# Kernel tuning notes

Hardware: AMD Instinct MI355X
Metric: run time of the kernel (lower is better)

## Reference

```python
import jax, jax.numpy as jnp
import numpy as np

B, C, H, W = 4, 128, 64, 64
HEADS = 4
GROUPS = 32
EPS = 1e-5


def setup_inputs() -> dict:
    key = jax.random.key(0)
    ks = jax.random.split(key, 7)
    x = jax.random.normal(ks[0], (B, C, H, W), jnp.float32)
    gn_gamma = 1.0 + 0.1 * jax.random.normal(ks[1], (C,), jnp.float32)
    gn_beta = 0.1 * jax.random.normal(ks[2], (C,), jnp.float32)
    # 1x1 convs stored as [out_ch, in_ch]
    w_qkv = jax.random.normal(ks[3], (3 * C, C), jnp.float32) / np.sqrt(C).astype(np.float32)
    b_qkv = 0.02 * jax.random.normal(ks[4], (3 * C,), jnp.float32)
    # proj_out is zero-init in the original; use small random weights so the
    # full math path (not just the residual) is exercised.
    w_proj = jax.random.normal(ks[5], (C, C), jnp.float32) / np.sqrt(C).astype(np.float32)
    b_proj = 0.02 * jax.random.normal(ks[6], (C,), jnp.float32)
    return {"x": x, "gn_gamma": gn_gamma, "gn_beta": gn_beta,
            "w_qkv": w_qkv, "b_qkv": b_qkv, "w_proj": w_proj, "b_proj": b_proj}


def reference(x, gn_gamma, gn_beta, w_qkv, b_qkv, w_proj, b_proj):
    b, c, h, w = x.shape
    # GroupNorm(32, C, affine=True)
    xg = x.reshape(b, GROUPS, c // GROUPS, h, w)
    mean = xg.mean(axis=(2, 3, 4), keepdims=True)
    var = xg.var(axis=(2, 3, 4), keepdims=True)
    hn = ((xg - mean) * jax.lax.rsqrt(var + EPS)).reshape(b, c, h, w)
    hn = hn * gn_gamma[None, :, None, None] + gn_beta[None, :, None, None]
    # 1x1 conv -> qkv: [B, 3C, H, W]
    qkv = jnp.einsum('bchw,oc->bohw', hn, w_qkv) + b_qkv[None, :, None, None]
    L = h * w
    qkv = qkv.reshape(b, 3 * c, L)
    q, k, v = jnp.split(qkv, 3, axis=1)  # each [B, C, L]
    ch = c // HEADS
    scale = 1.0 / np.sqrt(np.sqrt(ch)).astype(np.float32)
    qh = (q * scale).reshape(b * HEADS, ch, L)
    kh = (k * scale).reshape(b * HEADS, ch, L)
    vh = v.reshape(b * HEADS, ch, L)
    # full [B*heads, L, L] score matrix (as in the original einsum path)
    weight = jnp.einsum('bct,bcs->bts', qh, kh)
    weight = jax.nn.softmax(weight.astype(jnp.float32), axis=-1).astype(qkv.dtype)
    a = jnp.einsum('bts,bcs->bct', weight, vh).reshape(b, c, h, w)
    out = jnp.einsum('bchw,oc->bohw', a, w_proj) + b_proj[None, :, None, None]
    return x + out
```

## Files before the change

kernel.cpp:

```cpp
#include <hip/hip_runtime.h>
#include <math.h>

#define B_ 4
#define C_ 128
#define L_ 4096
#define EPS_ 1e-5f

typedef __attribute__((ext_vector_type(8))) short short8;
typedef __attribute__((ext_vector_type(4))) float f32x4;
typedef __attribute__((ext_vector_type(16))) float f32x16;

static __device__ __forceinline__ unsigned short f2bf(float f) {
  union { float f; unsigned u; } v; v.f = f;
  return (unsigned short)((v.u + 0x7FFFu + ((v.u >> 16) & 1u)) >> 16);
}
static __device__ __forceinline__ f32x4 fzero() {
  f32x4 z; z[0] = 0.f; z[1] = 0.f; z[2] = 0.f; z[3] = 0.f; return z;
}
static __device__ __forceinline__ f32x16 zero16() {
  f32x16 z;
#pragma unroll
  for (int i = 0; i < 16; ++i) z[i] = 0.f;
  return z;
}
static __device__ __forceinline__ float fexp2(float x) {
  return __builtin_amdgcn_exp2f(x);
}
static __device__ __forceinline__ unsigned cvtpk(float lo, float hi) {
  unsigned r;
  asm("v_cvt_pk_bf16_f32 %0, %1, %2" : "=v"(r) : "v"(lo), "v"(hi));
  return r;
}
#define PLSWAP(a, b) asm("v_permlane32_swap_b32 %0, %1" : "+v"(a), "+v"(b))


__global__ __launch_bounds__(256) void gn_prep(const float* __restrict__ x,
                                               float* __restrict__ mean,
                                               float* __restrict__ rstd,
                                               const float* __restrict__ wqkv,
                                               const float* __restrict__ bqkv,
                                               const float* __restrict__ wproj,
                                               unsigned short* __restrict__ wqkv_bf,
                                               unsigned short* __restrict__ wproj_bf,
                                               float* __restrict__ bqkv_s) {
  int bx = blockIdx.x;
  int tid = threadIdx.x;
  if (bx < 128) {
    int g = bx & 31, b = bx >> 5;
    const f32x4* p4 = (const f32x4*)(x + (size_t)(b * C_ + g * 4) * L_);
    float s = 0.f, sq = 0.f;
#pragma unroll
    for (int i = 0; i < 16; ++i) {
      f32x4 v = p4[tid + i * 256];
      s += v[0] + v[1] + v[2] + v[3];
      sq += v[0]*v[0] + v[1]*v[1] + v[2]*v[2] + v[3]*v[3];
    }
#pragma unroll
    for (int m = 1; m < 64; m <<= 1) { s += __shfl_xor(s, m, 64); sq += __shfl_xor(sq, m, 64); }
    __shared__ float ls[8];
    int w = tid >> 6;
    if ((tid & 63) == 0) { ls[w] = s; ls[4 + w] = sq; }
    __syncthreads();
    if (tid == 0) {
      float S = ls[0] + ls[1] + ls[2] + ls[3];
      float Q = ls[4] + ls[5] + ls[6] + ls[7];
      float mu = S * (1.f / 16384.f);
      float var = Q * (1.f / 16384.f) - mu * mu;
      mean[b * 32 + g] = mu;
      rstd[b * 32 + g] = rsqrtf(var + EPS_);
    }
  } else {
    const float SC = 0.42044820762685725f * 1.2011224087864498f;
    int i = (bx - 128) * 256 + tid;
    if (i < 49152) {
      int o = i >> 7;
      wqkv_bf[i] = f2bf(wqkv[i] * (o < 256 ? SC : 1.f));
    } else if (i < 65536) {
      wproj_bf[i - 49152] = f2bf(wproj[i - 49152]);
    } else if (i < 65920) {
      int o = i - 65536;
      bqkv_s[o] = bqkv[o] * (o < 256 ? SC : 1.f);
    }
  }
}

__global__ __launch_bounds__(256) void qkv_gemm(const float* __restrict__ x,
                                                const float* __restrict__ gamma,
                                                const float* __restrict__ beta,
                                                const float* __restrict__ mean,
                                                const float* __restrict__ rstd,
                                                const unsigned short* __restrict__ wqkv_bf,
                                                const float* __restrict__ bqkv_s,
                                                unsigned short* __restrict__ qbuf,
                                                char* __restrict__ kf,
                                                char* __restrict__ vf) {
  __shared__ char lds[64 * 256];
  int b = blockIdx.y;
  int pos0 = blockIdx.x * 64;
  int tid = threadIdx.x;

#pragma unroll
  for (int it = 0; it < 4; ++it) {
    int pi = it * 256 + tid;
    int c = (pi >> 4) * 2;
    int pl = (pi & 15) * 4;
    const float* xc = x + (size_t)(b * C_ + c) * L_ + pos0 + pl;
    f32x4 v0 = *(const f32x4*)xc;
    f32x4 v1 = *(const f32x4*)(xc + L_);
    int g = c >> 2;
    float rs = rstd[b * 32 + g], mu = mean[b * 32 + g];
    float A0 = rs * gamma[c],     B0 = beta[c]     - mu * A0;
    float A1 = rs * gamma[c + 1], B1 = beta[c + 1] - mu * A1;
#pragma unroll
    for (int i = 0; i < 4; ++i) {
      int row = pl + i;
      unsigned u = cvtpk(v0[i] * A0 + B0, v1[i] * A1 + B1);
      *(unsigned*)(lds + row * 256 + ((c * 2) ^ ((row & 7) << 4))) = u;
    }
  }
  __syncthreads();

  int l = tid & 63, w = tid >> 6;
  int ln = l & 15, g4 = l >> 4;
  int lrow = w * 16 + ln;

  short8 afrag[4];
#pragma unroll
  for (int kc = 0; kc < 4; ++kc) {
    int col2 = (kc * 32 + g4 * 8) * 2;
    afrag[kc] = *(const short8*)(lds + lrow * 256 + (col2 ^ ((lrow & 7) << 4)));
  }

  f32x4 acc[24];
#pragma unroll
  for (int nt = 0; nt < 24; ++nt) acc[nt] = fzero();
#pragma unroll
  for (int nt = 0; nt < 24; ++nt) {
#pragma unroll
    for (int kc = 0; kc < 4; ++kc) {
      short8 bfrag = *(const short8*)(wqkv_bf + (size_t)(nt * 16 + ln) * 128 + kc * 32 + g4 * 8);
      acc[nt] = __builtin_amdgcn_mfma_f32_16x16x32_bf16(afrag[kc], bfrag, acc[nt], 0, 0, 0);
    }
  }

  int posb = pos0 + w * 16 + g4 * 4;
  int s_ = posb >> 5;
#pragma unroll
  for (int nt = 0; nt < 24; ++nt) {
    int o = nt * 16 + ln;
    float bias = bqkv_s[o];
    unsigned u01 = cvtpk(acc[nt][0] + bias, acc[nt][1] + bias);
    unsigned u23 = cvtpk(acc[nt][2] + bias, acc[nt][3] + bias);
    if (o < 128) {
      int bh = b * 4 + (o >> 5);
      unsigned short* p = qbuf + ((size_t)bh * L_ + posb) * 32 + (o & 31);
      p[0]  = (unsigned short)u01; p[32] = (unsigned short)(u01 >> 16);
      p[64] = (unsigned short)u23; p[96] = (unsigned short)(u23 >> 16);
    } else if (o < 256) {
      int o2 = o - 128;
      int bh = b * 4 + (o2 >> 5);
      int d = o2 & 31;
      int hi_ = (d >> 3) & 1, blk_ = d >> 4, j_ = d & 7;
      int lq0 = posb & 31;
      char* base = kf + (size_t)bh * 262144 + s_ * 2048 + blk_ * 1024 + j_ * 2
                 + (hi_ * 32 + lq0) * 16;
      *(unsigned short*)(base)      = (unsigned short)u01;
      *(unsigned short*)(base + 16) = (unsigned short)(u01 >> 16);
      *(unsigned short*)(base + 32) = (unsigned short)u23;
      *(unsigned short*)(base + 48) = (unsigned short)(u23 >> 16);
    } else {
      int ch = o - 256;
      int bh = b * 4 + (ch >> 5);
      int d = ch & 31;
      int r5 = posb & 31;
      int hi_ = (r5 >> 3) & 1, blk_ = (r5 >> 4) & 1, j0 = r5 & 7;
      char* addr = vf + (size_t)bh * 262144 + s_ * 2048 + blk_ * 1024
                 + (hi_ * 32 + d) * 16 + j0 * 2;
      uint2 val; val.x = u01; val.y = u23;
      *(uint2*)addr = val;
    }
  }
}

#define COMPUTE(KA0, KA1, VA, VB)                                                 \
  {                                                                               \
    f32x16 sv = __builtin_amdgcn_mfma_f32_32x32x16_bf16(KA0, qf0, ZERO, 0, 0, 0); \
    sv = __builtin_amdgcn_mfma_f32_32x32x16_bf16(KA1, qf1, sv, 0, 0, 0);          \
    float p[16];                                                                  \
    _Pragma("unroll") for (int i = 0; i < 16; ++i) p[i] = fexp2(sv[i]);           \
    unsigned u0 = cvtpk(p[0], p[1]),   u1 = cvtpk(p[2], p[3]);                    \
    unsigned u2 = cvtpk(p[4], p[5]),   u3 = cvtpk(p[6], p[7]);                    \
    unsigned u4 = cvtpk(p[8], p[9]),   u5 = cvtpk(p[10], p[11]);                  \
    unsigned u6 = cvtpk(p[12], p[13]), u7 = cvtpk(p[14], p[15]);                  \
    PLSWAP(u0, u2); PLSWAP(u1, u3); PLSWAP(u4, u6); PLSWAP(u5, u7);               \
    union { unsigned uu[4]; short8 s8; } pa, pb;                                  \
    pa.uu[0] = u0; pa.uu[1] = u1; pa.uu[2] = u2; pa.uu[3] = u3;                   \
    pb.uu[0] = u4; pb.uu[1] = u5; pb.uu[2] = u6; pb.uu[3] = u7;                   \
    acc  = __builtin_amdgcn_mfma_f32_32x32x16_bf16(VA, pa.s8, acc, 0, 0, 0);      \
    acc  = __builtin_amdgcn_mfma_f32_32x32x16_bf16(VB, pb.s8, acc, 0, 0, 0);      \
    lacc = __builtin_amdgcn_mfma_f32_32x32x16_bf16(ONESF, pa.s8, lacc, 0, 0, 0);  \
    lacc = __builtin_amdgcn_mfma_f32_32x32x16_bf16(ONESF, pb.s8, lacc, 0, 0, 0);  \
  }

__global__ __launch_bounds__(512, 4) void attn_g(const unsigned short* __restrict__ qbuf,
                                                 const char* __restrict__ kf,
                                                 const char* __restrict__ vf,
                                                 unsigned short* __restrict__ at) {
  __shared__ float parts[6][17][64];
  const int bh = blockIdx.x;
  const int tid = threadIdx.x;
  const int l = tid & 63, w = tid >> 6;
  const int lq = l & 31, hi = l >> 5;
  const int qg = w & 1, kvh = w >> 1;
  const int lo16 = l * 16;

  const unsigned short* qb = qbuf + (size_t)bh * L_ * 32;
  const char* kp = kf + (size_t)bh * 262144 + (size_t)kvh * 32 * 2048 + lo16;
  const char* vp = vf + (size_t)bh * 262144 + (size_t)kvh * 32 * 2048 + lo16;

  const int qbase = blockIdx.y * 64 + qg * 32;
  short8 qf0 = *(const short8*)(qb + (size_t)(qbase + lq) * 32 + hi * 8);
  short8 qf1 = *(const short8*)(qb + (size_t)(qbase + lq) * 32 + 16 + hi * 8);

  short8 ONESF;
#pragma unroll
  for (int i = 0; i < 8; ++i) ONESF[i] = (short)0x3F80;
  const f32x16 ZERO = zero16();
  f32x16 acc = zero16();
  f32x16 lacc = zero16();

  short8 kA0 = *(const short8*)(kp);
  short8 kA1 = *(const short8*)(kp + 1024);
  short8 vA0 = *(const short8*)(vp);
  short8 vA1 = *(const short8*)(vp + 1024);
  short8 kB0 = *(const short8*)(kp + 2048);
  short8 kB1 = *(const short8*)(kp + 3072);
  short8 vB0 = *(const short8*)(vp + 2048);
  short8 vB1 = *(const short8*)(vp + 3072);

  for (int s = 0; s < 32; s += 2) {
    const int adv = (s < 30) ? 4096 : 0;
    kp += adv; vp += adv;
    COMPUTE(kA0, kA1, vA0, vA1);
    kA0 = *(const short8*)(kp);
    kA1 = *(const short8*)(kp + 1024);
    vA0 = *(const short8*)(vp);
    vA1 = *(const short8*)(vp + 1024);
    COMPUTE(kB0, kB1, vB0, vB1);
    kB0 = *(const short8*)(kp + 2048);
    kB1 = *(const short8*)(kp + 3072);
    vB0 = *(const short8*)(vp + 2048);
    vB1 = *(const short8*)(vp + 3072);
  }

  if (w >= 2) {
    const int slot = w - 2;
#pragma unroll
    for (int r = 0; r < 16; ++r) parts[slot][r][l] = acc[r];
    parts[slot][16][l] = lacc[0];
  }
  __syncthreads();
  if (w < 2) {
    float lsum = lacc[0];
#pragma unroll
    for (int j = 0; j < 3; ++j) {
      const int slot = qg + j * 2;
#pragma unroll
      for (int r = 0; r < 16; ++r) acc[r] += parts[slot][r][l];
      lsum += parts[slot][16][l];
    }
    float inv = 1.f / lsum;
    int b = bh >> 2, h = bh & 3;
    size_t base = ((size_t)b * L_ + qbase + lq) * 128 + h * 32;
#pragma unroll
    for (int rq = 0; rq < 4; ++rq) {
      unsigned w0 = cvtpk(acc[rq * 4 + 0] * inv, acc[rq * 4 + 1] * inv);
      unsigned w1 = cvtpk(acc[rq * 4 + 2] * inv, acc[rq * 4 + 3] * inv);
      uint2 val; val.x = w0; val.y = w1;
      *(uint2*)(at + base + rq * 8 + hi * 4) = val;
    }
  }
}

__global__ __launch_bounds__(256) void proj_residual(const float* __restrict__ x,
                                                     const unsigned short* __restrict__ at,
                                                     const unsigned short* __restrict__ wproj_bf,
                                                     const float* __restrict__ bproj,
                                                     float* __restrict__ out) {
  int b = blockIdx.y;
  int pos0 = blockIdx.x * 64;
  int tid = threadIdx.x;
  int l = tid & 63, w = tid >> 6;
  int ln = l & 15, g4 = l >> 4;
  int posw = pos0 + w * 16;

  short8 bfrag[4];
#pragma unroll
  for (int kc = 0; kc < 4; ++kc)
    bfrag[kc] = *(const short8*)(at + ((size_t)b * L_ + posw + ln) * 128 + kc * 32 + g4 * 8);

  f32x4 acc[8];
#pragma unroll
  for (int mt = 0; mt < 8; ++mt) acc[mt] = fzero();
#pragma unroll
  for (int mt = 0; mt < 8; ++mt) {
#pragma unroll
    for (int kc = 0; kc < 4; ++kc) {
      short8 afrag = *(const short8*)(wproj_bf + (size_t)(mt * 16 + ln) * 128 + kc * 32 + g4 * 8);
      acc[mt] = __builtin_amdgcn_mfma_f32_16x16x32_bf16(afrag, bfrag[kc], acc[mt], 0, 0, 0);
    }
  }
#pragma unroll
  for (int mt = 0; mt < 8; ++mt)
#pragma unroll
    for (int r = 0; r < 4; ++r) {
      int o = mt * 16 + g4 * 4 + r;
      int pos = posw + ln;
      size_t idx = ((size_t)b * C_ + o) * L_ + pos;
      out[idx] = x[idx] + acc[mt][r] + bproj[o];
    }
}

extern "C" void kernel_launch(void* const* d_in, const int* in_sizes, int n_in,
                              void* d_out, int out_size, void* d_ws, size_t ws_size,
                              hipStream_t stream) {
  const float* x     = (const float*)d_in[0];
  const float* gamma = (const float*)d_in[1];
  const float* beta  = (const float*)d_in[2];
  const float* wqkv  = (const float*)d_in[3];
  const float* bqkv  = (const float*)d_in[4];
  const float* wproj = (const float*)d_in[5];
  const float* bproj = (const float*)d_in[6];
  float* out = (float*)d_out;

  char* ws = (char*)d_ws;
  float* mean   = (float*)(ws + 0);
  float* rstd   = (float*)(ws + 512);
  float* bqkv_s = (float*)(ws + 1024);
  unsigned short* wqkv_bf  = (unsigned short*)(ws + 4096);
  unsigned short* wproj_bf = (unsigned short*)(ws + 102400);
  unsigned short* qbuf = (unsigned short*)(ws + 135168);
  char* kf = ws + 135168 + 4194304;
  char* vf = ws + 135168 + 2 * 4194304;
  unsigned short* at = (unsigned short*)(ws + 135168 + 3 * 4194304);

  gn_prep<<<dim3(386), 256, 0, stream>>>(x, mean, rstd, wqkv, bqkv, wproj,
                                         wqkv_bf, wproj_bf, bqkv_s);
  qkv_gemm<<<dim3(64, 4), 256, 0, stream>>>(x, gamma, beta, mean, rstd, wqkv_bf, bqkv_s,
                                            qbuf, kf, vf);
  attn_g<<<dim3(16, 64), 512, 0, stream>>>(qbuf, kf, vf, at);
  proj_residual<<<dim3(64, 4), 256, 0, stream>>>(x, at, wproj_bf, bproj, out);
}
```

Before: 90.12 us.

## Process two query tiles per wave in attention and sum softmax denominators in VALU

Each wave now handles both 32-row query tiles of the block against a quarter of the keys, so every K/V fragment loaded from global memory is used twice. Blocks shrink from 8 to 4 waves. The row-sum of exponentials is now accumulated with scalar adds plus a cross-half shuffle instead of extra MFMAs against a ones vector, which removes a third of the matrix instructions. The trade-off is higher register pressure from two accumulators and four Q fragments, a different occupancy hint, and a simpler one-step-ahead prefetch loop that is not unrolled.

Result: faster. 81.48 us (median of 3 runs) (-9.6%).

```diff
diff --git a/kernel.cpp b/kernel.cpp
--- a/kernel.cpp
+++ b/kernel.cpp
@@ -182,12 +182,12 @@
   }
 }
 
-#define COMPUTE(KA0, KA1, VA, VB)                                                 \
+#define SOFTMAX_PV(SV, LSUM, ACC)                                                 \
   {                                                                               \
-    f32x16 sv = __builtin_amdgcn_mfma_f32_32x32x16_bf16(KA0, qf0, ZERO, 0, 0, 0); \
-    sv = __builtin_amdgcn_mfma_f32_32x32x16_bf16(KA1, qf1, sv, 0, 0, 0);          \
     float p[16];                                                                  \
-    _Pragma("unroll") for (int i = 0; i < 16; ++i) p[i] = fexp2(sv[i]);           \
+    _Pragma("unroll") for (int i = 0; i < 16; ++i) p[i] = fexp2((SV)[i]);         \
+    LSUM += (((p[0]+p[1])+(p[2]+p[3])) + ((p[4]+p[5])+(p[6]+p[7])))               \
+          + (((p[8]+p[9])+(p[10]+p[11])) + ((p[12]+p[13])+(p[14]+p[15])));        \
     unsigned u0 = cvtpk(p[0], p[1]),   u1 = cvtpk(p[2], p[3]);                    \
     unsigned u2 = cvtpk(p[4], p[5]),   u3 = cvtpk(p[6], p[7]);                    \
     unsigned u4 = cvtpk(p[8], p[9]),   u5 = cvtpk(p[10], p[11]);                  \
@@ -196,88 +196,95 @@
     union { unsigned uu[4]; short8 s8; } pa, pb;                                  \
     pa.uu[0] = u0; pa.uu[1] = u1; pa.uu[2] = u2; pa.uu[3] = u3;                   \
     pb.uu[0] = u4; pb.uu[1] = u5; pb.uu[2] = u6; pb.uu[3] = u7;                   \
-    acc  = __builtin_amdgcn_mfma_f32_32x32x16_bf16(VA, pa.s8, acc, 0, 0, 0);      \
-    acc  = __builtin_amdgcn_mfma_f32_32x32x16_bf16(VB, pb.s8, acc, 0, 0, 0);      \
-    lacc = __builtin_amdgcn_mfma_f32_32x32x16_bf16(ONESF, pa.s8, lacc, 0, 0, 0);  \
-    lacc = __builtin_amdgcn_mfma_f32_32x32x16_bf16(ONESF, pb.s8, lacc, 0, 0, 0);  \
-  }
-
-__global__ __launch_bounds__(512, 4) void attn_g(const unsigned short* __restrict__ qbuf,
+    ACC = __builtin_amdgcn_mfma_f32_32x32x16_bf16(vC0, pa.s8, ACC, 0, 0, 0);      \
+    ACC = __builtin_amdgcn_mfma_f32_32x32x16_bf16(vC1, pb.s8, ACC, 0, 0, 0);      \
+  }
+
+__global__ __launch_bounds__(256, 3) void attn_g(const unsigned short* __restrict__ qbuf,
                                                  const char* __restrict__ kf,
                                                  const char* __restrict__ vf,
                                                  unsigned short* __restrict__ at) {
-  __shared__ float parts[6][17][64];
+  __shared__ float parts[3][34][64];
   const int bh = blockIdx.x;
   const int tid = threadIdx.x;
   const int l = tid & 63, w = tid >> 6;
   const int lq = l & 31, hi = l >> 5;
-  const int qg = w & 1, kvh = w >> 1;
   const int lo16 = l * 16;
 
   const unsigned short* qb = qbuf + (size_t)bh * L_ * 32;
-  const char* kp = kf + (size_t)bh * 262144 + (size_t)kvh * 32 * 2048 + lo16;
-  const char* vp = vf + (size_t)bh * 262144 + (size_t)kvh * 32 * 2048 + lo16;
-
-  const int qbase = blockIdx.y * 64 + qg * 32;
-  short8 qf0 = *(const short8*)(qb + (size_t)(qbase + lq) * 32 + hi * 8);
-  short8 qf1 = *(const short8*)(qb + (size_t)(qbase + lq) * 32 + 16 + hi * 8);
-
-  short8 ONESF;
-#pragma unroll
-  for (int i = 0; i < 8; ++i) ONESF[i] = (short)0x3F80;
+  const char* kp = kf + (size_t)bh * 262144 + (size_t)w * 65536 + lo16;
+  const char* vp = vf + (size_t)bh * 262144 + (size_t)w * 65536 + lo16;
+
+  const int qbase = blockIdx.y * 64;
+  short8 qfA0 = *(const short8*)(qb + (size_t)(qbase + lq) * 32 + hi * 8);
+  short8 qfA1 = *(const short8*)(qb + (size_t)(qbase + lq) * 32 + 16 + hi * 8);
+  short8 qfB0 = *(const short8*)(qb + (size_t)(qbase + 32 + lq) * 32 + hi * 8);
+  short8 qfB1 = *(const short8*)(qb + (size_t)(qbase + 32 + lq) * 32 + 16 + hi * 8);
+
   const f32x16 ZERO = zero16();
-  f32x16 acc = zero16();
-  f32x16 lacc = zero16();
-
-  short8 kA0 = *(const short8*)(kp);
-  short8 kA1 = *(const short8*)(kp + 1024);
-  short8 vA0 = *(const short8*)(vp);
-  short8 vA1 = *(const short8*)(vp + 1024);
-  short8 kB0 = *(const short8*)(kp + 2048);
-  short8 kB1 = *(const short8*)(kp + 3072);
-  short8 vB0 = *(const short8*)(vp + 2048);
-  short8 vB1 = *(const short8*)(vp + 3072);
-
-  for (int s = 0; s < 32; s += 2) {
-    const int adv = (s < 30) ? 4096 : 0;
-    kp += adv; vp += adv;
-    COMPUTE(kA0, kA1, vA0, vA1);
-    kA0 = *(const short8*)(kp);
-    kA1 = *(const short8*)(kp + 1024);
-    vA0 = *(const short8*)(vp);
-    vA1 = *(const short8*)(vp + 1024);
-    COMPUTE(kB0, kB1, vB0, vB1);
-    kB0 = *(const short8*)(kp + 2048);
-    kB1 = *(const short8*)(kp + 3072);
-    vB0 = *(const short8*)(vp + 2048);
-    vB1 = *(const short8*)(vp + 3072);
-  }
-
-  if (w >= 2) {
-    const int slot = w - 2;
-#pragma unroll
-    for (int r = 0; r < 16; ++r) parts[slot][r][l] = acc[r];
-    parts[slot][16][l] = lacc[0];
+  f32x16 accA = zero16();
+  f32x16 accB = zero16();
+  float lsumA = 0.f, lsumB = 0.f;
+
+  short8 kC0 = *(const short8*)(kp);
+  short8 kC1 = *(const short8*)(kp + 1024);
+  short8 vC0 = *(const short8*)(vp);
+  short8 vC1 = *(const short8*)(vp + 1024);
+
+#pragma unroll 1
+  for (int s = 0; s < 32; ++s) {
+    short8 kN0 = *(const short8*)(kp + 2048);
+    short8 kN1 = *(const short8*)(kp + 3072);
+    short8 vN0 = *(const short8*)(vp + 2048);
+    short8 vN1 = *(const short8*)(vp + 3072);
+    f32x16 sA = __builtin_amdgcn_mfma_f32_32x32x16_bf16(kC0, qfA0, ZERO, 0, 0, 0);
+    sA = __builtin_amdgcn_mfma_f32_32x32x16_bf16(kC1, qfA1, sA, 0, 0, 0);
+    f32x16 sB = __builtin_amdgcn_mfma_f32_32x32x16_bf16(kC0, qfB0, ZERO, 0, 0, 0);
+    sB = __builtin_amdgcn_mfma_f32_32x32x16_bf16(kC1, qfB1, sB, 0, 0, 0);
+    SOFTMAX_PV(sA, lsumA, accA);
+    SOFTMAX_PV(sB, lsumB, accB);
+    kC0 = kN0; kC1 = kN1; vC0 = vN0; vC1 = vN1;
+    kp += 2048; vp += 2048;
+  }
+
+  if (w > 0) {
+    const int slot = w - 1;
+#pragma unroll
+    for (int r = 0; r < 16; ++r) {
+      parts[slot][r][l] = accA[r];
+      parts[slot][16 + r][l] = accB[r];
+    }
+    parts[slot][32][l] = lsumA;
+    parts[slot][33][l] = lsumB;
   }
   __syncthreads();
-  if (w < 2) {
-    float lsum = lacc[0];
+  if (w == 0) {
 #pragma unroll
     for (int j = 0; j < 3; ++j) {
-      const int slot = qg + j * 2;
-#pragma unroll
-      for (int r = 0; r < 16; ++r) acc[r] += parts[slot][r][l];
-      lsum += parts[slot][16][l];
-    }
-    float inv = 1.f / lsum;
+#pragma unroll
+      for (int r = 0; r < 16; ++r) {
+        accA[r] += parts[j][r][l];
+        accB[r] += parts[j][16 + r][l];
+      }
+      lsumA += parts[j][32][l];
+      lsumB += parts[j][33][l];
+    }
+    lsumA += __shfl_xor(lsumA, 32, 64);
+    lsumB += __shfl_xor(lsumB, 32, 64);
+    float invA = 1.f / lsumA;
+    float invB = 1.f / lsumB;
     int b = bh >> 2, h = bh & 3;
-    size_t base = ((size_t)b * L_ + qbase + lq) * 128 + h * 32;
+    size_t baseA = ((size_t)b * L_ + qbase + lq) * 128 + h * 32;
+    size_t baseB = baseA + 32 * 128;
 #pragma unroll
     for (int rq = 0; rq < 4; ++rq) {
-      unsigned w0 = cvtpk(acc[rq * 4 + 0] * inv, acc[rq * 4 + 1] * inv);
-      unsigned w1 = cvtpk(acc[rq * 4 + 2] * inv, acc[rq * 4 + 3] * inv);
-      uint2 val; val.x = w0; val.y = w1;
-      *(uint2*)(at + base + rq * 8 + hi * 4) = val;
+      uint2 valA, valB;
+      valA.x = cvtpk(accA[rq * 4 + 0] * invA, accA[rq * 4 + 1] * invA);
+      valA.y = cvtpk(accA[rq * 4 + 2] * invA, accA[rq * 4 + 3] * invA);
+      valB.x = cvtpk(accB[rq * 4 + 0] * invB, accB[rq * 4 + 1] * invB);
+      valB.y = cvtpk(accB[rq * 4 + 2] * invB, accB[rq * 4 + 3] * invB);
+      *(uint2*)(at + baseA + rq * 8 + hi * 4) = valA;
+      *(uint2*)(at + baseB + rq * 8 + hi * 4) = valB;
     }
   }
 }
@@ -348,6 +355,6 @@
                                          wqkv_bf, wproj_bf, bqkv_s);
   qkv_gemm<<<dim3(64, 4), 256, 0, stream>>>(x, gamma, beta, mean, rstd, wqkv_bf, bqkv_s,
                                             qbuf, kf, vf);
-  attn_g<<<dim3(16, 64), 512, 0, stream>>>(qbuf, kf, vf, at);
+  attn_g<<<dim3(16, 64), 256, 0, stream>>>(qbuf, kf, vf, at);
   proj_residual<<<dim3(64, 4), 256, 0, stream>>>(x, at, wproj_bf, bproj, out);
 }
```
